# Performance work log

Hardware: AMD Instinct MI355X
Metric: run time of the kernel (lower is better)

## Reference

```python
import jax, jax.numpy as jnp
import numpy as np

D = 1024      # d_model
H = 16        # n_head
DH = D // H   # d_head = 64
DFF = 4 * D   # 4096
B, T = 1, 4096
EPS = 1e-5


def _layernorm(x, scale, bias):
    mu = jnp.mean(x, axis=-1, keepdims=True)
    var = jnp.mean(jnp.square(x - mu), axis=-1, keepdims=True)
    return (x - mu) * jax.lax.rsqrt(var + EPS) * scale + bias


def setup_inputs() -> dict:
    key = jax.random.key(0)
    ks = jax.random.split(key, 8)
    s = 0.02
    return {
        "x": jax.random.normal(ks[0], (B, T, D), jnp.float32),
        "ln1_scale": jnp.ones((D,), jnp.float32),
        "ln1_bias": jnp.zeros((D,), jnp.float32),
        "W_attn": jax.random.normal(ks[1], (D, 3 * D), jnp.float32) * s,
        "b_attn": jnp.zeros((3 * D,), jnp.float32),
        "W_proj": jax.random.normal(ks[2], (D, D), jnp.float32) * s,
        "b_proj": jnp.zeros((D,), jnp.float32),
        "ln2_scale": jnp.ones((D,), jnp.float32),
        "ln2_bias": jnp.zeros((D,), jnp.float32),
        "W_fc": jax.random.normal(ks[3], (D, DFF), jnp.float32) * s,
        "b_fc": jnp.zeros((DFF,), jnp.float32),
        "W_fc2": jax.random.normal(ks[4], (DFF, D), jnp.float32) * s,
        "b_fc2": jnp.zeros((D,), jnp.float32),
    }


def reference(x, ln1_scale, ln1_bias, W_attn, b_attn, W_proj, b_proj,
              ln2_scale, ln2_bias, W_fc, b_fc, W_fc2, b_fc2):
    Bx, Tx, C = x.shape
    # --- attention branch ---
    h = _layernorm(x, ln1_scale, ln1_bias)
    qkv = h @ W_attn + b_attn                      # [B,T,3D]
    q, k, v = jnp.split(qkv, 3, axis=-1)
    q = q.reshape(Bx, Tx, H, DH).transpose(0, 2, 1, 3)  # [B,H,T,dh]
    k = k.reshape(Bx, Tx, H, DH).transpose(0, 2, 1, 3)
    v = v.reshape(Bx, Tx, H, DH).transpose(0, 2, 1, 3)
    att = jnp.einsum('bhqd,bhkd->bhqk', q, k) * (1.0 / jnp.sqrt(DH))
    causal = jnp.tril(jnp.ones((Tx, Tx), dtype=jnp.bool_))[None, None]
    att = jnp.where(causal, att, -jnp.inf)
    att = jax.nn.softmax(att, axis=-1)
    y = jnp.einsum('bhqk,bhkd->bhqd', att, v)      # [B,H,T,dh]
    y = y.transpose(0, 2, 1, 3).reshape(Bx, Tx, C)
    y = y @ W_proj + b_proj
    x = x + y
    # --- MLP branch ---
    h2 = _layernorm(x, ln2_scale, ln2_bias)
    m = jax.nn.gelu(h2 @ W_fc + b_fc)              # approximate gelu (flax default)
    m = m @ W_fc2 + b_fc2
    return x + m
```

## Files before the change

### kernel.cpp

```cpp
#include <hip/hip_runtime.h>
#include <hip/hip_bf16.h>

typedef short bf16x8 __attribute__((ext_vector_type(8)));
typedef float f32x4 __attribute__((ext_vector_type(4)));
typedef unsigned short u16;
typedef unsigned int u32;

#define TSEQ 4096
#define DMODEL 1024
#define NHEAD 16
#define DHEAD 64
#define DFF 4096

__device__ __forceinline__ u16 f2bf(float f) {
    u32 u = __builtin_bit_cast(u32, f);
    u32 lsb = (u >> 16) & 1u;
    u += 0x7fffu + lsb;
    return (u16)(u >> 16);
}

__device__ __forceinline__ float exp2_hw(float x) {
    float r;
    asm("v_exp_f32 %0, %1" : "=v"(r) : "v"(x));
    return r;
}

__device__ __forceinline__ float rcp_hw(float x) {
    float r;
    asm("v_rcp_f32 %0, %1" : "=v"(r) : "v"(x));
    return r;
}

__device__ __forceinline__ u32 cvt_pk_bf16(float a, float b) {
    u32 r;
    asm("v_cvt_pk_bf16_f32 %0, %1, %2" : "=v"(r) : "v"(a), "v"(b));
    return r;
}

__device__ __forceinline__ void gload_lds16(const u16* g, u16* l) {
    __builtin_amdgcn_global_load_lds(
        (const __attribute__((address_space(1))) u32*)g,
        (__attribute__((address_space(3))) u32*)l, 16, 0, 0);
}

__global__ __launch_bounds__(256)
void transpose_cast_kernel(const float* __restrict__ W, u16* __restrict__ Wt, int K, int N)
{
    __shared__ float tile[64][65];
    const int t = threadIdx.x;
    const int c = t & 63, r4 = t >> 6;
    const int col0 = blockIdx.x * 64;
    const int row0 = blockIdx.y * 64;
#pragma unroll
    for (int p = 0; p < 16; p++) {
        const int r = 4 * p + r4;
        tile[r][c] = W[(size_t)(row0 + r) * N + col0 + c];
    }
    __syncthreads();
#pragma unroll
    for (int p = 0; p < 16; p++) {
        const int r = 4 * p + r4;
        Wt[(size_t)(col0 + r) * K + row0 + c] = f2bf(tile[c][r]);
    }
}

__global__ __launch_bounds__(256)
void v_transpose_kernel(const u16* __restrict__ qkv, u16* __restrict__ Vtg)
{
    __shared__ u16 tile[64][72];
    const int t = threadIdx.x;
    const int hh = blockIdx.y, t0 = blockIdx.x * 64;
#pragma unroll
    for (int p = 0; p < 2; p++) {
        const int L = p * 2048 + t * 8;
        const int r = L >> 6, c = L & 63;
        const bf16x8 v = *(const bf16x8*)(qkv + (size_t)(t0 + r) * 3072 + 2048 + hh * 64 + c);
#pragma unroll
        for (int i = 0; i < 8; i++) tile[c + i][r] = (u16)v[i];
    }
    __syncthreads();
#pragma unroll
    for (int p = 0; p < 2; p++) {
        const int L = p * 2048 + t * 8;
        const int d = L >> 6, c = L & 63;
        bf16x8 v;
#pragma unroll
        for (int i = 0; i < 8; i++) v[i] = (short)tile[d][c + i];
        *(bf16x8*)(Vtg + (size_t)(hh * 64 + d) * TSEQ + t0 + c) = v;
    }
}

__global__ __launch_bounds__(256)
void ln_kernel(const float* __restrict__ x, const float* __restrict__ sc,
               const float* __restrict__ bi, u16* __restrict__ out)
{
    const int lane = threadIdx.x & 63;
    const int row = blockIdx.x * 4 + (threadIdx.x >> 6);
    const float* xr = x + (size_t)row * DMODEL;
    float4 v[4];
    float s = 0.f, s2 = 0.f;
#pragma unroll
    for (int q = 0; q < 4; q++) {
        v[q] = *(const float4*)(xr + 4 * (lane + 64 * q));
        s  += v[q].x + v[q].y + v[q].z + v[q].w;
        s2 += v[q].x * v[q].x + v[q].y * v[q].y + v[q].z * v[q].z + v[q].w * v[q].w;
    }
#pragma unroll
    for (int off = 1; off < 64; off <<= 1) {
        s  += __shfl_xor(s, off);
        s2 += __shfl_xor(s2, off);
    }
    const float mu = s * (1.f / DMODEL);
    const float rstd = rsqrtf(s2 * (1.f / DMODEL) - mu * mu + 1e-5f);
#pragma unroll
    for (int q = 0; q < 4; q++) {
        const int c = 4 * (lane + 64 * q);
        const float4 scv = *(const float4*)(sc + c);
        const float4 biv = *(const float4*)(bi + c);
        ushort4 ov;
        ov.x = f2bf((v[q].x - mu) * rstd * scv.x + biv.x);
        ov.y = f2bf((v[q].y - mu) * rstd * scv.y + biv.y);
        ov.z = f2bf((v[q].z - mu) * rstd * scv.z + biv.z);
        ov.w = f2bf((v[q].w - mu) * rstd * scv.w + biv.w);
        *(ushort4*)(out + (size_t)row * DMODEL + c) = ov;
    }
}

template<int BN, int GELU_F, int OUT_BF16, int HAS_RES>
__global__ __launch_bounds__(256)
void gemm_kernel(const u16* __restrict__ A, const u16* __restrict__ Bt,
                 const float* __restrict__ bias, const float* __restrict__ res,
                 u16* __restrict__ outb, float* __restrict__ outf,
                 int M, int N, int K)
{
    constexpr int MI = (BN == 128) ? 4 : 2;
    __shared__ u16 Alds[128 * 32];
    __shared__ u16 Blds[BN * 32];
    const int t = threadIdx.x;
    const int lane = t & 63, w = t >> 6;
    const int g = lane >> 4, fr = lane & 15;
    const int m0 = blockIdx.y * 128, n0 = blockIdx.x * BN;
    const int rowbase = (BN == 128) ? (w >> 1) * 64 : w * 32;
    const int colbase = (BN == 128) ? (w & 1) * 64 : 0;

    f32x4 zero4 = {0.f, 0.f, 0.f, 0.f};
    f32x4 acc[MI][4];
#pragma unroll
    for (int i = 0; i < MI; i++)
#pragma unroll
        for (int j = 0; j < 4; j++) acc[i][j] = zero4;

    const int E0 = (w * 2 + 0) * 512 + lane * 8;
    const int E1 = (w * 2 + 1) * 512 + lane * 8;
    const int EB = t * 8;

    for (int k0 = 0; k0 < K; k0 += 32) {
        __syncthreads();
        gload_lds16(A + (size_t)(m0 + (E0 >> 5)) * K + k0 + (E0 & 31), Alds + E0);
        gload_lds16(A + (size_t)(m0 + (E1 >> 5)) * K + k0 + (E1 & 31), Alds + E1);
        if constexpr (BN == 128) {
            gload_lds16(Bt + (size_t)(n0 + (E0 >> 5)) * K + k0 + (E0 & 31), Blds + E0);
            gload_lds16(Bt + (size_t)(n0 + (E1 >> 5)) * K + k0 + (E1 & 31), Blds + E1);
        } else {
            gload_lds16(Bt + (size_t)(n0 + (EB >> 5)) * K + k0 + (EB & 31), Blds + EB);
        }
        __syncthreads();

        bf16x8 af[MI], bfr[4];
#pragma unroll
        for (int i = 0; i < MI; i++)
            af[i] = *(const bf16x8*)(Alds + (rowbase + i * 16 + fr) * 32 + g * 8);
#pragma unroll
        for (int j = 0; j < 4; j++)
            bfr[j] = *(const bf16x8*)(Blds + (colbase + j * 16 + fr) * 32 + g * 8);
#pragma unroll
        for (int i = 0; i < MI; i++)
#pragma unroll
            for (int j = 0; j < 4; j++)
                acc[i][j] = __builtin_amdgcn_mfma_f32_16x16x32_bf16(af[i], bfr[j], acc[i][j], 0, 0, 0);
    }

#pragma unroll
    for (int j = 0; j < 4; j++) {
        const int col = n0 + colbase + j * 16 + fr;
        const float bv = bias[col];
#pragma unroll
        for (int i = 0; i < MI; i++) {
#pragma unroll
            for (int r = 0; r < 4; r++) {
                const int row = m0 + rowbase + i * 16 + g * 4 + r;
                float v = acc[i][j][r] + bv;
                if (GELU_F) {
                    const float q = 0.7978845608028654f * (v + 0.044715f * v * v * v);
                    const float e = exp2_hw(fminf(q, 30.f) * 2.8853900817779268f);
                    v = v * e * rcp_hw(e + 1.0f);
                }
                if (HAS_RES) v += res[(size_t)row * N + col];
                if (OUT_BF16) outb[(size_t)row * N + col] = f2bf(v);
                else          outf[(size_t)row * N + col] = v;
            }
        }
    }
}

__device__ __forceinline__ void softmax_update(
    const f32x4 st[4], bool diag, int klim, int g, int fr,
    float& mrow, float& lrow, f32x4 o[4], u16* Pl)
{
    const float ninf = -__builtin_inff();
    const float C = 0.125f * 1.4426950408889634f;
    float av[4][4];
#pragma unroll
    for (int ct = 0; ct < 4; ct++)
#pragma unroll
        for (int r = 0; r < 4; r++) {
            float aa = st[ct][r];
            if (diag && (ct * 16 + g * 4 + r) > klim) aa = ninf;
            av[ct][r] = aa;
        }
    float m0 = fmaxf(fmaxf(av[0][0], av[0][1]), fmaxf(av[0][2], av[0][3]));
    float m1 = fmaxf(fmaxf(av[1][0], av[1][1]), fmaxf(av[1][2], av[1][3]));
    float m2 = fmaxf(fmaxf(av[2][0], av[2][1]), fmaxf(av[2][2], av[2][3]));
    float m3 = fmaxf(fmaxf(av[3][0], av[3][1]), fmaxf(av[3][2], av[3][3]));
    float vm = fmaxf(fmaxf(m0, m1), fmaxf(m2, m3));
    vm = fmaxf(vm, __shfl_xor(vm, 16));
    vm = fmaxf(vm, __shfl_xor(vm, 32));
    const float mn = (vm <= mrow + 64.f) ? mrow : vm;
    const float mnC = mn * C;
    float rs = 0.f;
#pragma unroll
    for (int ct = 0; ct < 4; ct++) {
        const float p0 = exp2_hw(__builtin_fmaf(av[ct][0], C, -mnC));
        const float p1 = exp2_hw(__builtin_fmaf(av[ct][1], C, -mnC));
        const float p2 = exp2_hw(__builtin_fmaf(av[ct][2], C, -mnC));
        const float p3 = exp2_hw(__builtin_fmaf(av[ct][3], C, -mnC));
        rs += (p0 + p1) + (p2 + p3);
        uint2 pk;
        pk.x = cvt_pk_bf16(p0, p1);
        pk.y = cvt_pk_bf16(p2, p3);
        const int chunk = ct * 2 + (g >> 1);
        const int addr = fr * 64 + ((chunk ^ (fr & 7)) * 8) + (g & 1) * 4;
        *(uint2*)(Pl + addr) = pk;
    }
    rs += __shfl_xor(rs, 16);
    rs += __shfl_xor(rs, 32);
    const float sc = exp2_hw((mrow - mn) * C);
    lrow = __builtin_fmaf(lrow, sc, rs);
    const bool nores = (mn == mrow);
    mrow = mn;
    if (!__all(nores)) {
        float scb[4];
#pragma unroll
        for (int j = 0; j < 4; j++) scb[j] = __shfl(sc, g * 4 + j);
#pragma unroll
        for (int dt = 0; dt < 4; dt++)
#pragma unroll
            for (int j = 0; j < 4; j++) o[dt][j] *= scb[j];
    }
}

__global__ __launch_bounds__(512, 4)
void attn_kernel(const u16* __restrict__ qkv, const u16* __restrict__ Vtg,
                 u16* __restrict__ y)
{
    __shared__ u16 Klds[2][128 * 64];
    __shared__ u16 Vlds[2][64 * 128];
    __shared__ u16 Plds[8][16 * 64];
    const int t = threadIdx.x, lane = t & 63, w = t >> 6;
    const int g = lane >> 4, fr = lane & 15;
    const int wv = w & 3, grp = w >> 2;
    const int hh = blockIdx.y;
    const int ii = blockIdx.x;
    const int ntB = 64 - ii;
    const int qAw = ii * 64 + wv * 16;
    const int qBw = (63 - ii) * 64 + wv * 16;

    bf16x8 aqA[2], aqB[2];
#pragma unroll
    for (int s = 0; s < 2; s++) {
        aqA[s] = *(const bf16x8*)(qkv + (size_t)(qAw + fr) * 3072 + hh * 64 + s * 32 + g * 8);
        aqB[s] = *(const bf16x8*)(qkv + (size_t)(qBw + fr) * 3072 + hh * 64 + s * 32 + g * 8);
    }

    f32x4 zero4 = {0.f, 0.f, 0.f, 0.f};
    f32x4 oA[4] = {zero4, zero4, zero4, zero4};
    f32x4 oB[4] = {zero4, zero4, zero4, zero4};
    const float ninf = -__builtin_inff();
    float mA = ninf, lA = 0.f, mB = ninf, lB = 0.f;

    const int cK0 = t, cK1 = t + 512;
    const int rK0 = cK0 >> 3, jK0 = (cK0 & 7) ^ (rK0 & 7);
    const int rK1 = cK1 >> 3, jK1 = (cK1 & 7) ^ (rK1 & 7);
    const int rv0 = cK0 >> 4, cj0 = cK0 & 15;
    const int jv0 = (cj0 & 8) | ((cj0 & 7) ^ (rv0 & 7));
    const int rv1 = cK1 >> 4, cj1 = cK1 & 15;
    const int jv1 = (cj1 & 8) | ((cj1 & 7) ^ (rv1 & 7));
    const u16* gk0 = qkv + (size_t)rK0 * 3072 + 1024 + hh * 64 + jK0 * 8;
    const u16* gk1 = qkv + (size_t)rK1 * 3072 + 1024 + hh * 64 + jK1 * 8;
    const u16* gv0 = Vtg + (size_t)(hh * 64 + rv0) * TSEQ + jv0 * 8;
    const u16* gv1 = Vtg + (size_t)(hh * 64 + rv1) * TSEQ + jv1 * 8;

#define STAGE(buf, k0) do { \
        gload_lds16(gk0 + (size_t)(k0) * 3072, Klds[buf] + cK0 * 8); \
        gload_lds16(gk1 + (size_t)(k0) * 3072, Klds[buf] + cK1 * 8); \
        gload_lds16(gv0 + (k0), Vlds[buf] + cK0 * 8); \
        gload_lds16(gv1 + (k0), Vlds[buf] + cK1 * 8); \
    } while (0)

    const int nIter = (65 - ii) >> 1;
    STAGE(0, 0);

    int cur = 0;
    for (int j = 0; j < nIter; j++) {
        __syncthreads();
        if (j + 1 < nIter) STAGE(cur ^ 1, (j + 1) * 128);

        const int kt = 2 * j + grp;
        const bool aB = kt < ntB;
        const bool aA = kt <= ii;
        if (aB | aA) {
            const u16* Kl = Klds[cur] + grp * (64 * 64);
            const u16* Vl = Vlds[cur];
            const int klim = wv * 16 + fr;

            f32x4 stA[4] = {zero4, zero4, zero4, zero4};
            f32x4 stB[4] = {zero4, zero4, zero4, zero4};
#pragma unroll
            for (int ct = 0; ct < 4; ct++) {
#pragma unroll
                for (int ds = 0; ds < 2; ds++) {
                    const bf16x8 bk = *(const bf16x8*)(Kl + (ct * 16 + fr) * 64 + (((ds * 4 + g) ^ (fr & 7)) * 8));
                    if (aB) stB[ct] = __builtin_amdgcn_mfma_f32_16x16x32_bf16(bk, aqB[ds], stB[ct], 0, 0, 0);
                    if (aA) stA[ct] = __builtin_amdgcn_mfma_f32_16x16x32_bf16(bk, aqA[ds], stA[ct], 0, 0, 0);
                }
            }

            if (aB) {
                softmax_update(stB, kt == ntB - 1, klim, g, fr, mB, lB, oB, Plds[w]);
                __builtin_amdgcn_s_waitcnt(0xc07f);
#pragma unroll
                for (int kkh = 0; kkh < 2; kkh++) {
                    const bf16x8 pa = *(const bf16x8*)(&Plds[w][fr * 64 + (((kkh * 4 + g) ^ (fr & 7)) * 8)]);
#pragma unroll
                    for (int dt = 0; dt < 4; dt++) {
                        const int cc = grp * 8 + kkh * 4 + g;
                        const bf16x8 bv = *(const bf16x8*)(Vl + (dt * 16 + fr) * 128 + (((cc & 8) | ((cc & 7) ^ (fr & 7))) * 8));
                        oB[dt] = __builtin_amdgcn_mfma_f32_16x16x32_bf16(pa, bv, oB[dt], 0, 0, 0);
                    }
                }
            }
            if (aA) {
                softmax_update(stA, kt == ii, klim, g, fr, mA, lA, oA, Plds[w]);
                __builtin_amdgcn_s_waitcnt(0xc07f);
#pragma unroll
                for (int kkh = 0; kkh < 2; kkh++) {
                    const bf16x8 pa = *(const bf16x8*)(&Plds[w][fr * 64 + (((kkh * 4 + g) ^ (fr & 7)) * 8)]);
#pragma unroll
                    for (int dt = 0; dt < 4; dt++) {
                        const int cc = grp * 8 + kkh * 4 + g;
                        const bf16x8 bv = *(const bf16x8*)(Vl + (dt * 16 + fr) * 128 + (((cc & 8) | ((cc & 7) ^ (fr & 7))) * 8));
                        oA[dt] = __builtin_amdgcn_mfma_f32_16x16x32_bf16(pa, bv, oA[dt], 0, 0, 0);
                    }
                }
            }
        }
        cur ^= 1;
    }
#undef STAGE

    __syncthreads();
    float* Of = (float*)&Klds[0][0];
    float2* Ml = (float2*)&Vlds[0][0];
    const float C = 0.125f * 1.4426950408889634f;
    if (grp == 1) {
#pragma unroll
        for (int dt = 0; dt < 4; dt++)
#pragma unroll
            for (int jq = 0; jq < 4; jq++) {
                Of[((wv * 2 + 0) * 16 + g * 4 + jq) * 64 + dt * 16 + fr] = oA[dt][jq];
                Of[((wv * 2 + 1) * 16 + g * 4 + jq) * 64 + dt * 16 + fr] = oB[dt][jq];
            }
        if (g == 0) {
            Ml[(wv * 2 + 0) * 16 + fr] = make_float2(mA, lA);
            Ml[(wv * 2 + 1) * 16 + fr] = make_float2(mB, lB);
        }
    }
    __syncthreads();
    if (grp == 0) {
#pragma unroll
        for (int jq = 0; jq < 4; jq++) {
            {
                const float m0 = __shfl(mA, g * 4 + jq), l0 = __shfl(lA, g * 4 + jq);
                const float2 ml1 = Ml[(wv * 2 + 0) * 16 + g * 4 + jq];
                const float mm = fmaxf(m0, ml1.x);
                const float s0 = exp2_hw((m0 - mm) * C);
                const float s1 = exp2_hw((ml1.x - mm) * C);
                const float rl = rcp_hw(__builtin_fmaf(l0, s0, ml1.y * s1));
#pragma unroll
                for (int dt = 0; dt < 4; dt++) {
                    const float o1 = Of[((wv * 2 + 0) * 16 + g * 4 + jq) * 64 + dt * 16 + fr];
                    y[(size_t)(qAw + g * 4 + jq) * DMODEL + hh * 64 + dt * 16 + fr] =
                        f2bf((oA[dt][jq] * s0 + o1 * s1) * rl);
                }
            }
            {
                const float m0 = __shfl(mB, g * 4 + jq), l0 = __shfl(lB, g * 4 + jq);
                const float2 ml1 = Ml[(wv * 2 + 1) * 16 + g * 4 + jq];
                const float mm = fmaxf(m0, ml1.x);
                const float s0 = exp2_hw((m0 - mm) * C);
                const float s1 = exp2_hw((ml1.x - mm) * C);
                const float rl = rcp_hw(__builtin_fmaf(l0, s0, ml1.y * s1));
#pragma unroll
                for (int dt = 0; dt < 4; dt++) {
                    const float o1 = Of[((wv * 2 + 1) * 16 + g * 4 + jq) * 64 + dt * 16 + fr];
                    y[(size_t)(qBw + g * 4 + jq) * DMODEL + hh * 64 + dt * 16 + fr] =
                        f2bf((oB[dt][jq] * s0 + o1 * s1) * rl);
                }
            }
        }
    }
}

extern "C" void kernel_launch(void* const* d_in, const int* in_sizes, int n_in,
                              void* d_out, int out_size, void* d_ws, size_t ws_size,
                              hipStream_t stream)
{
    const float* x      = (const float*)d_in[0];
    const float* ln1_s  = (const float*)d_in[1];
    const float* ln1_b  = (const float*)d_in[2];
    const float* W_attn = (const float*)d_in[3];
    const float* b_attn = (const float*)d_in[4];
    const float* W_proj = (const float*)d_in[5];
    const float* b_proj = (const float*)d_in[6];
    const float* ln2_s  = (const float*)d_in[7];
    const float* ln2_b  = (const float*)d_in[8];
    const float* W_fc   = (const float*)d_in[9];
    const float* b_fc   = (const float*)d_in[10];
    const float* W_fc2  = (const float*)d_in[11];
    const float* b_fc2  = (const float*)d_in[12];
    float* out = (float*)d_out;

    char* ws = (char*)d_ws;
    u16* WtAttn = (u16*)ws; ws += (size_t)3072 * 1024 * 2;
    u16* WtProj = (u16*)ws; ws += (size_t)1024 * 1024 * 2;
    u16* WtFc   = (u16*)ws; ws += (size_t)4096 * 1024 * 2;
    u16* WtFc2  = (u16*)ws; ws += (size_t)1024 * 4096 * 2;
    u16* bufA   = (u16*)ws; ws += (size_t)4096 * 1024 * 2;
    u16* bufB   = (u16*)ws; ws += (size_t)4096 * 4096 * 2;
    float* x1   = (float*)ws; ws += (size_t)4096 * 1024 * 4;
    u16* Vtg    = (u16*)x1;

    transpose_cast_kernel<<<dim3(3072 / 64, 1024 / 64), 256, 0, stream>>>(W_attn, WtAttn, 1024, 3072);
    transpose_cast_kernel<<<dim3(1024 / 64, 1024 / 64), 256, 0, stream>>>(W_proj, WtProj, 1024, 1024);
    transpose_cast_kernel<<<dim3(4096 / 64, 1024 / 64), 256, 0, stream>>>(W_fc,   WtFc,   1024, 4096);
    transpose_cast_kernel<<<dim3(1024 / 64, 4096 / 64), 256, 0, stream>>>(W_fc2,  WtFc2,  4096, 1024);

    ln_kernel<<<TSEQ / 4, 256, 0, stream>>>(x, ln1_s, ln1_b, bufA);
    gemm_kernel<128, 0, 1, 0><<<dim3(3072 / 128, 4096 / 128), 256, 0, stream>>>(
        bufA, WtAttn, b_attn, nullptr, bufB, nullptr, 4096, 3072, 1024);
    v_transpose_kernel<<<dim3(TSEQ / 64, NHEAD), 256, 0, stream>>>(bufB, Vtg);
    attn_kernel<<<dim3(32, NHEAD), 512, 0, stream>>>(bufB, Vtg, bufA);
    gemm_kernel<64, 0, 0, 1><<<dim3(1024 / 64, 4096 / 128), 256, 0, stream>>>(
        bufA, WtProj, b_proj, x, nullptr, x1, 4096, 1024, 1024);

    ln_kernel<<<TSEQ / 4, 256, 0, stream>>>(x1, ln2_s, ln2_b, bufA);
    gemm_kernel<128, 1, 1, 0><<<dim3(4096 / 128, 4096 / 128), 256, 0, stream>>>(
        bufA, WtFc, b_fc, nullptr, bufB, nullptr, 4096, 4096, 1024);
    gemm_kernel<64, 0, 0, 1><<<dim3(1024 / 64, 4096 / 128), 256, 0, stream>>>(
        bufB, WtFc2, b_fc2, x1, nullptr, out, 4096, 1024, 4096);
}
```

Before: 308.2 us.

## Use BK=64 XOR-swizzled LDS tiles and split-K for FC2 GEMM

Result: faster. 289.3 us (-6.1%).

```diff
diff --git a/kernel.cpp b/kernel.cpp
--- a/kernel.cpp
+++ b/kernel.cpp
@@ -126,22 +126,25 @@
     }
 }
 
-template<int BN, int GELU_F, int OUT_BF16, int HAS_RES>
+template<int BN, int GELU_F, int OUT_BF16, int HAS_RES, int HAS_BIAS>
 __global__ __launch_bounds__(256)
-void gemm_kernel(const u16* __restrict__ A, const u16* __restrict__ Bt,
+void gemm_kernel(const u16* __restrict__ A, int lda,
+                 const u16* __restrict__ Bt, int ldb,
                  const float* __restrict__ bias, const float* __restrict__ res,
-                 u16* __restrict__ outb, float* __restrict__ outf,
-                 int M, int N, int K)
+                 u16* __restrict__ outb, float* __restrict__ outf0,
+                 float* __restrict__ outf1, int M, int N, int Kblk)
 {
     constexpr int MI = (BN == 128) ? 4 : 2;
-    __shared__ u16 Alds[128 * 32];
-    __shared__ u16 Blds[BN * 32];
+    __shared__ u16 Alds[128 * 64];
+    __shared__ u16 Blds[BN * 64];
     const int t = threadIdx.x;
     const int lane = t & 63, w = t >> 6;
     const int g = lane >> 4, fr = lane & 15;
     const int m0 = blockIdx.y * 128, n0 = blockIdx.x * BN;
+    const size_t koff = (size_t)blockIdx.z * Kblk;
     const int rowbase = (BN == 128) ? (w >> 1) * 64 : w * 32;
     const int colbase = (BN == 128) ? (w & 1) * 64 : 0;
+    float* outf = blockIdx.z ? outf1 : outf0;
 
     f32x4 zero4 = {0.f, 0.f, 0.f, 0.f};
     f32x4 acc[MI][4];
@@ -150,40 +153,44 @@
 #pragma unroll
         for (int j = 0; j < 4; j++) acc[i][j] = zero4;
 
-    const int E0 = (w * 2 + 0) * 512 + lane * 8;
-    const int E1 = (w * 2 + 1) * 512 + lane * 8;
-    const int EB = t * 8;
-
-    for (int k0 = 0; k0 < K; k0 += 32) {
+    for (int k0 = 0; k0 < Kblk; k0 += 64) {
         __syncthreads();
-        gload_lds16(A + (size_t)(m0 + (E0 >> 5)) * K + k0 + (E0 & 31), Alds + E0);
-        gload_lds16(A + (size_t)(m0 + (E1 >> 5)) * K + k0 + (E1 & 31), Alds + E1);
-        if constexpr (BN == 128) {
-            gload_lds16(Bt + (size_t)(n0 + (E0 >> 5)) * K + k0 + (E0 & 31), Blds + E0);
-            gload_lds16(Bt + (size_t)(n0 + (E1 >> 5)) * K + k0 + (E1 & 31), Blds + E1);
-        } else {
-            gload_lds16(Bt + (size_t)(n0 + (EB >> 5)) * K + k0 + (EB & 31), Blds + EB);
+#pragma unroll
+        for (int p = 0; p < 4; p++) {
+            const int c = p * 256 + t;
+            const int r = c >> 3, j = (c & 7) ^ (r & 7);
+            gload_lds16(A + (size_t)(m0 + r) * lda + koff + k0 + j * 8, Alds + c * 8);
+        }
+#pragma unroll
+        for (int p = 0; p < (BN == 128 ? 4 : 2); p++) {
+            const int c = p * 256 + t;
+            const int r = c >> 3, j = (c & 7) ^ (r & 7);
+            gload_lds16(Bt + (size_t)(n0 + r) * ldb + koff + k0 + j * 8, Blds + c * 8);
         }
         __syncthreads();
 
-        bf16x8 af[MI], bfr[4];
-#pragma unroll
-        for (int i = 0; i < MI; i++)
-            af[i] = *(const bf16x8*)(Alds + (rowbase + i * 16 + fr) * 32 + g * 8);
-#pragma unroll
-        for (int j = 0; j < 4; j++)
-            bfr[j] = *(const bf16x8*)(Blds + (colbase + j * 16 + fr) * 32 + g * 8);
-#pragma unroll
-        for (int i = 0; i < MI; i++)
+#pragma unroll
+        for (int ks = 0; ks < 2; ks++) {
+            bf16x8 af[MI], bfr[4];
+#pragma unroll
+            for (int i = 0; i < MI; i++)
+                af[i] = *(const bf16x8*)(Alds + (rowbase + i * 16 + fr) * 64 + (((ks * 4 + g) ^ (fr & 7)) * 8));
 #pragma unroll
             for (int j = 0; j < 4; j++)
-                acc[i][j] = __builtin_amdgcn_mfma_f32_16x16x32_bf16(af[i], bfr[j], acc[i][j], 0, 0, 0);
+                bfr[j] = *(const bf16x8*)(Blds + (colbase + j * 16 + fr) * 64 + (((ks * 4 + g) ^ (fr & 7)) * 8));
+#pragma unroll
+            for (int i = 0; i < MI; i++)
+#pragma unroll
+                for (int j = 0; j < 4; j++)
+                    acc[i][j] = __builtin_amdgcn_mfma_f32_16x16x32_bf16(af[i], bfr[j], acc[i][j], 0, 0, 0);
+        }
     }
 
 #pragma unroll
     for (int j = 0; j < 4; j++) {
         const int col = n0 + colbase + j * 16 + fr;
-        const float bv = bias[col];
+        float bv = 0.f;
+        if (HAS_BIAS) bv = bias[col];
 #pragma unroll
         for (int i = 0; i < MI; i++) {
 #pragma unroll
@@ -201,6 +208,23 @@
             }
         }
     }
+}
+
+__global__ __launch_bounds__(256)
+void fc2_merge_kernel(float* __restrict__ out, const float* __restrict__ part,
+                      const float* __restrict__ x1, const float* __restrict__ bias)
+{
+    const int i = blockIdx.x * 256 + threadIdx.x;
+    const float4 o = ((const float4*)out)[i];
+    const float4 p = ((const float4*)part)[i];
+    const float4 r = ((const float4*)x1)[i];
+    const float4 b = ((const float4*)bias)[i & 255];
+    float4 v;
+    v.x = o.x + p.x + r.x + b.x;
+    v.y = o.y + p.y + r.y + b.y;
+    v.z = o.z + p.z + r.z + b.z;
+    v.w = o.w + p.w + r.w + b.w;
+    ((float4*)out)[i] = v;
 }
 
 __device__ __forceinline__ void softmax_update(
@@ -449,6 +473,7 @@
     u16* bufB   = (u16*)ws; ws += (size_t)4096 * 4096 * 2;
     float* x1   = (float*)ws; ws += (size_t)4096 * 1024 * 4;
     u16* Vtg    = (u16*)x1;
+    float* P0   = (float*)d_ws;
 
     transpose_cast_kernel<<<dim3(3072 / 64, 1024 / 64), 256, 0, stream>>>(W_attn, WtAttn, 1024, 3072);
     transpose_cast_kernel<<<dim3(1024 / 64, 1024 / 64), 256, 0, stream>>>(W_proj, WtProj, 1024, 1024);
@@ -456,16 +481,17 @@
     transpose_cast_kernel<<<dim3(1024 / 64, 4096 / 64), 256, 0, stream>>>(W_fc2,  WtFc2,  4096, 1024);
 
     ln_kernel<<<TSEQ / 4, 256, 0, stream>>>(x, ln1_s, ln1_b, bufA);
-    gemm_kernel<128, 0, 1, 0><<<dim3(3072 / 128, 4096 / 128), 256, 0, stream>>>(
-        bufA, WtAttn, b_attn, nullptr, bufB, nullptr, 4096, 3072, 1024);
+    gemm_kernel<128, 0, 1, 0, 1><<<dim3(24, 32, 1), 256, 0, stream>>>(
+        bufA, 1024, WtAttn, 1024, b_attn, nullptr, bufB, nullptr, nullptr, 4096, 3072, 1024);
     v_transpose_kernel<<<dim3(TSEQ / 64, NHEAD), 256, 0, stream>>>(bufB, Vtg);
     attn_kernel<<<dim3(32, NHEAD), 512, 0, stream>>>(bufB, Vtg, bufA);
-    gemm_kernel<64, 0, 0, 1><<<dim3(1024 / 64, 4096 / 128), 256, 0, stream>>>(
-        bufA, WtProj, b_proj, x, nullptr, x1, 4096, 1024, 1024);
+    gemm_kernel<64, 0, 0, 1, 1><<<dim3(16, 32, 1), 256, 0, stream>>>(
+        bufA, 1024, WtProj, 1024, b_proj, x, nullptr, x1, nullptr, 4096, 1024, 1024);
 
     ln_kernel<<<TSEQ / 4, 256, 0, stream>>>(x1, ln2_s, ln2_b, bufA);
-    gemm_kernel<128, 1, 1, 0><<<dim3(4096 / 128, 4096 / 128), 256, 0, stream>>>(
-        bufA, WtFc, b_fc, nullptr, bufB, nullptr, 4096, 4096, 1024);
-    gemm_kernel<64, 0, 0, 1><<<dim3(1024 / 64, 4096 / 128), 256, 0, stream>>>(
-        bufB, WtFc2, b_fc2, x1, nullptr, out, 4096, 1024, 4096);
-}
+    gemm_kernel<128, 1, 1, 0, 1><<<dim3(32, 32, 1), 256, 0, stream>>>(
+        bufA, 1024, WtFc, 1024, b_fc, nullptr, bufB, nullptr, nullptr, 4096, 4096, 1024);
+    gemm_kernel<128, 0, 0, 0, 0><<<dim3(8, 32, 2), 256, 0, stream>>>(
+        bufB, 4096, WtFc2, 4096, nullptr, nullptr, nullptr, P0, out, 4096, 1024, 2048);
+    fc2_merge_kernel<<<4096, 256, 0, stream>>>(out, P0, x1, b_fc2);
+}
```
